# Kernel tuning notes

Hardware: AMD Instinct MI355X
Metric: run time of the kernel (lower is better)

The kernel has to match this reference:

```python
import jax, jax.numpy as jnp
import numpy as np

B, T, S, H, V = 4, 512, 1024, 768, 50257

def setup_inputs() -> dict:
    key = jax.random.key(0)
    k1, k2, k3, k4, k5, k6 = jax.random.split(key, 6)
    input_ids_to_copy = jax.random.randint(k1, (B, S), 0, V)
    cross_attentions = jax.random.uniform(k2, (B, T, S), dtype=jnp.float32)
    # normalize like attention weights
    cross_attentions = cross_attentions / jnp.sum(cross_attentions, axis=-1, keepdims=True)
    src_hidden_states = jax.random.normal(k3, (B, S, H), dtype=jnp.float32)
    tgt_hidden_states = jax.random.normal(k4, (B, T, H), dtype=jnp.float32)
    # p_gen_head = Linear(2H, 1) + Sigmoid
    W_pgen = jax.random.normal(k5, (2 * H, 1), dtype=jnp.float32) * (1.0 / np.sqrt(2 * H))
    b_pgen = jnp.zeros((1,), dtype=jnp.float32)
    return {
        "input_ids_to_copy": input_ids_to_copy,
        "cross_attentions": cross_attentions,
        "src_hidden_states": src_hidden_states,
        "tgt_hidden_states": tgt_hidden_states,
        "W_pgen": W_pgen,
        "b_pgen": b_pgen,
    }

def _copy_logits(attn_bts, ids_bs, vocab_size):
    # logits[b,t,v] = sum_s attn[b,t,s] * (ids[b,s] == v)
    # Efficient scatter-add over source positions instead of one-hot + matmul.
    def per_batch(attn_ts, ids_s):
        # attn_ts: [T,S], ids_s: [S] -> segment_sum over S -> [V,T] -> [T,V]
        return jax.ops.segment_sum(attn_ts.T, ids_s, num_segments=vocab_size).T
    return jax.vmap(per_batch)(attn_bts, ids_bs)

def reference(input_ids_to_copy, cross_attentions, src_hidden_states,
              tgt_hidden_states, W_pgen, b_pgen):
    # context_vectors: [B,T,H]
    context_vectors = jnp.einsum('bts,bsh->bth', cross_attentions, src_hidden_states)
    total_states = jnp.concatenate((context_vectors, tgt_hidden_states), axis=-1)  # [B,T,2H]
    p_gen = jax.nn.sigmoid(total_states @ W_pgen + b_pgen)  # [B,T,1]
    logits = _copy_logits(cross_attentions, input_ids_to_copy, V)  # [B,T,V]
    return (p_gen, logits)
```

## Files before the change

### kernel.cpp

```cpp
#include <hip/hip_runtime.h>
#include <hip/hip_bf16.h>
#include <math.h>

#define BB 4
#define TT 512
#define SS 1024
#define HH 768
#define VV 50257
#define NW 1571
#define NWP 1600
#define NPROJ 1536

__global__ __launch_bounds__(256) void prep_kernel(
    const float* __restrict__ src, const float* __restrict__ tgt,
    const float* __restrict__ W, const float* __restrict__ bptr,
    const int* __restrict__ ids,
    float* __restrict__ src_proj, float* __restrict__ tgt_proj,
    unsigned* __restrict__ bm_g, unsigned* __restrict__ pre_g,
    unsigned short* __restrict__ rank_g)
{
    __shared__ unsigned bm[NW];
    __shared__ unsigned pre[NW];
    __shared__ unsigned scan[256];
    const int tid = threadIdx.x;

    if (blockIdx.x < NPROJ) {
        const int wave = tid >> 6;
        const int lane = tid & 63;
        const int row  = blockIdx.x * 4 + wave;

        const float* vec;
        const float* w;
        if (row < BB * SS) { vec = src + (size_t)row * HH;            w = W; }
        else               { vec = tgt + (size_t)(row - BB*SS) * HH;  w = W + HH; }
        const float4* v4 = (const float4*)vec;
        const float4* w4 = (const float4*)w;

        float acc = 0.f;
#pragma unroll
        for (int k = 0; k < 3; ++k) {
            float4 a = v4[k * 64 + lane];
            float4 b = w4[k * 64 + lane];
            acc += a.x * b.x + a.y * b.y + a.z * b.z + a.w * b.w;
        }
#pragma unroll
        for (int off = 32; off > 0; off >>= 1) acc += __shfl_down(acc, off);
        if (lane == 0) {
            if (row < BB * SS) src_proj[row] = acc;
            else               tgt_proj[row - BB * SS] = acc + bptr[0];
        }
        return;
    }

    const int b = blockIdx.x - NPROJ;

    for (int i = tid; i < NW; i += 256) bm[i] = 0u;
    __syncthreads();
    const int* idb = ids + b * SS;
    for (int s = tid; s < SS; s += 256) {
        const int v = idb[s];
        atomicOr(&bm[v >> 5], 1u << (v & 31));
    }
    __syncthreads();

    unsigned cnt[7];
    unsigned local = 0;
    const int w0 = tid * 7;
#pragma unroll
    for (int k = 0; k < 7; ++k) {
        const int w = w0 + k;
        cnt[k] = local;
        local += (w < NW) ? (unsigned)__popc(bm[w]) : 0u;
    }
    scan[tid] = local;
    __syncthreads();
    for (int off = 1; off < 256; off <<= 1) {
        const unsigned mine = scan[tid];
        const unsigned add  = (tid >= off) ? scan[tid - off] : 0u;
        __syncthreads();
        scan[tid] = mine + add;
        __syncthreads();
    }
    const unsigned excl = (tid > 0) ? scan[tid - 1] : 0u;
#pragma unroll
    for (int k = 0; k < 7; ++k) {
        const int w = w0 + k;
        if (w < NW) {
            const unsigned p = excl + cnt[k];
            pre[w] = p;
            pre_g[b * NWP + w] = p;
            bm_g[b * NWP + w]  = bm[w];
        }
    }
    __syncthreads();
    for (int s = tid; s < SS; s += 256) {
        const int v = idb[s];
        const unsigned w = (unsigned)v >> 5, bit = (unsigned)v & 31u;
        const unsigned r = pre[w] + (unsigned)__popc(bm[w] & ((1u << bit) - 1u));
        rank_g[b * SS + s] = (unsigned short)r;
    }
}

__device__ __forceinline__ float lut1(int v, const unsigned* bm,
                                      const unsigned* pre, const float* vals)
{
    const unsigned w = bm[v >> 5];
    const unsigned bit = (unsigned)v & 31u;
    if ((w >> bit) & 1u)
        return vals[pre[v >> 5] + (unsigned)__popc(w & ((1u << bit) - 1u))];
    return 0.f;
}

__global__ __launch_bounds__(256) void row_kernel(
    const float* __restrict__ attn,
    const float* __restrict__ src_proj,
    const float* __restrict__ tgt_proj,
    const unsigned* __restrict__ bm_g,
    const unsigned* __restrict__ pre_g,
    const unsigned short* __restrict__ rank_g,
    float* __restrict__ out)
{
    __shared__ unsigned bm[NW];
    __shared__ unsigned pre[NW];
    __shared__ float vals[SS];
    __shared__ float wsum[4];

    const int row = blockIdx.x;
    const int b   = row >> 9;
    const int tid = threadIdx.x;

    for (int i = tid; i < NW; i += 256) { bm[i] = bm_g[b*NWP+i]; pre[i] = pre_g[b*NWP+i]; }
    ((float4*)vals)[tid] = make_float4(0.f, 0.f, 0.f, 0.f);
    __syncthreads();

    const float4*  a4p = (const float4*)(attn + (size_t)row * SS);
    const float4*  sp4 = (const float4*)(src_proj + b * SS);
    const ushort4* r4p = (const ushort4*)(rank_g + b * SS);
    const float4  a = a4p[tid];
    const float4  p = sp4[tid];
    const ushort4 r = r4p[tid];
    atomicAdd(&vals[r.x], a.x);
    atomicAdd(&vals[r.y], a.y);
    atomicAdd(&vals[r.z], a.z);
    atomicAdd(&vals[r.w], a.w);
    float acc = a.x * p.x + a.y * p.y + a.z * p.z + a.w * p.w;
#pragma unroll
    for (int off = 32; off > 0; off >>= 1) acc += __shfl_down(acc, off);
    if ((tid & 63) == 0) wsum[tid >> 6] = acc;
    __syncthreads();
    if (tid == 0) {
        const float x = wsum[0] + wsum[1] + wsum[2] + wsum[3] + tgt_proj[row];
        out[row] = 1.f / (1.f + expf(-x));
    }

    float* logits = out + (BB * TT) + (size_t)row * VV;
    const int head = (int)(((16u - (unsigned)((uintptr_t)logits & 15u)) & 15u) >> 2);
    if (tid < head) logits[tid] = lut1(tid, bm, pre, vals);

    const int n4 = (VV - head) >> 2;
    float4* p4 = (float4*)(logits + head);
    for (int i = tid; i < n4; i += 256) {
        const int v0 = head + (i << 2);
        float4 o = make_float4(0.f, 0.f, 0.f, 0.f);
        const unsigned w  = bm[v0 >> 5];
        const unsigned sh = (unsigned)v0 & 31u;
        unsigned nib;
        if (sh <= 28u) {
            nib = (w >> sh) & 0xFu;
        } else {
            const unsigned hi = bm[(v0 >> 5) + 1];
            nib = ((w >> sh) | (hi << (32u - sh))) & 0xFu;
        }
        if (nib) {
            o.x = lut1(v0,     bm, pre, vals);
            o.y = lut1(v0 + 1, bm, pre, vals);
            o.z = lut1(v0 + 2, bm, pre, vals);
            o.w = lut1(v0 + 3, bm, pre, vals);
        }
        p4[i] = o;
    }
    const int done = head + (n4 << 2);
    for (int v = done + tid; v < VV; v += 256)
        logits[v] = lut1(v, bm, pre, vals);
}

extern "C" void kernel_launch(void* const* d_in, const int* in_sizes, int n_in,
                              void* d_out, int out_size, void* d_ws, size_t ws_size,
                              hipStream_t stream) {
    const int*   ids  = (const int*)d_in[0];
    const float* attn = (const float*)d_in[1];
    const float* src  = (const float*)d_in[2];
    const float* tgt  = (const float*)d_in[3];
    const float* W    = (const float*)d_in[4];
    const float* bp   = (const float*)d_in[5];

    float* out = (float*)d_out;

    float*          src_proj = (float*)d_ws;
    float*          tgt_proj = src_proj + BB * SS;
    unsigned*       bm_g     = (unsigned*)(tgt_proj + BB * TT);
    unsigned*       pre_g    = bm_g + BB * NWP;
    unsigned short* rank_g   = (unsigned short*)(pre_g + BB * NWP);

    prep_kernel<<<NPROJ + BB, 256, 0, stream>>>(
        src, tgt, W, bp, ids, src_proj, tgt_proj, bm_g, pre_g, rank_g);
    row_kernel<<<BB * TT, 256, 0, stream>>>(
        attn, src_proj, tgt_proj, bm_g, pre_g, rank_g, out);
}
```

Before: 465.6 us.

## Zero-fill logit rows and scatter unique source values instead of dense LUT

Result: slower. 497.9 us (+6.9%).

```diff
diff --git a/kernel.cpp b/kernel.cpp
--- a/kernel.cpp
+++ b/kernel.cpp
@@ -1,5 +1,4 @@
 #include <hip/hip_runtime.h>
-#include <hip/hip_bf16.h>
 #include <math.h>
 
 #define BB 4
@@ -8,15 +7,14 @@
 #define HH 768
 #define VV 50257
 #define NW 1571
-#define NWP 1600
 #define NPROJ 1536
+#define NROWS (BB * TT)
 
 __global__ __launch_bounds__(256) void prep_kernel(
     const float* __restrict__ src, const float* __restrict__ tgt,
     const float* __restrict__ W, const float* __restrict__ bptr,
     const int* __restrict__ ids,
     float* __restrict__ src_proj, float* __restrict__ tgt_proj,
-    unsigned* __restrict__ bm_g, unsigned* __restrict__ pre_g,
     unsigned short* __restrict__ rank_g)
 {
     __shared__ unsigned bm[NW];
@@ -85,12 +83,7 @@
 #pragma unroll
     for (int k = 0; k < 7; ++k) {
         const int w = w0 + k;
-        if (w < NW) {
-            const unsigned p = excl + cnt[k];
-            pre[w] = p;
-            pre_g[b * NWP + w] = p;
-            bm_g[b * NWP + w]  = bm[w];
-        }
+        if (w < NW) pre[w] = excl + cnt[k];
     }
     __syncthreads();
     for (int s = tid; s < SS; s += 256) {
@@ -101,27 +94,14 @@
     }
 }
 
-__device__ __forceinline__ float lut1(int v, const unsigned* bm,
-                                      const unsigned* pre, const float* vals)
-{
-    const unsigned w = bm[v >> 5];
-    const unsigned bit = (unsigned)v & 31u;
-    if ((w >> bit) & 1u)
-        return vals[pre[v >> 5] + (unsigned)__popc(w & ((1u << bit) - 1u))];
-    return 0.f;
-}
-
 __global__ __launch_bounds__(256) void row_kernel(
     const float* __restrict__ attn,
     const float* __restrict__ src_proj,
     const float* __restrict__ tgt_proj,
-    const unsigned* __restrict__ bm_g,
-    const unsigned* __restrict__ pre_g,
     const unsigned short* __restrict__ rank_g,
+    const int* __restrict__ ids,
     float* __restrict__ out)
 {
-    __shared__ unsigned bm[NW];
-    __shared__ unsigned pre[NW];
     __shared__ float vals[SS];
     __shared__ float wsum[4];
 
@@ -129,16 +109,12 @@
     const int b   = row >> 9;
     const int tid = threadIdx.x;
 
-    for (int i = tid; i < NW; i += 256) { bm[i] = bm_g[b*NWP+i]; pre[i] = pre_g[b*NWP+i]; }
     ((float4*)vals)[tid] = make_float4(0.f, 0.f, 0.f, 0.f);
     __syncthreads();
 
-    const float4*  a4p = (const float4*)(attn + (size_t)row * SS);
-    const float4*  sp4 = (const float4*)(src_proj + b * SS);
-    const ushort4* r4p = (const ushort4*)(rank_g + b * SS);
-    const float4  a = a4p[tid];
-    const float4  p = sp4[tid];
-    const ushort4 r = r4p[tid];
+    const float4  a = ((const float4*)(attn + (size_t)row * SS))[tid];
+    const float4  p = ((const float4*)(src_proj + b * SS))[tid];
+    const ushort4 r = ((const ushort4*)(rank_g + b * SS))[tid];
     atomicAdd(&vals[r.x], a.x);
     atomicAdd(&vals[r.y], a.y);
     atomicAdd(&vals[r.z], a.z);
@@ -147,41 +123,35 @@
 #pragma unroll
     for (int off = 32; off > 0; off >>= 1) acc += __shfl_down(acc, off);
     if ((tid & 63) == 0) wsum[tid >> 6] = acc;
+
+    float* lp = out + NROWS + (size_t)row * VV;
+    const int h = (4 - (row & 3)) & 3;
+    if (tid < h) lp[tid] = 0.f;
+    float4* lp4 = (float4*)(lp + h);
+    const int n4 = (VV - h) >> 2;
+    const float4 z4 = make_float4(0.f, 0.f, 0.f, 0.f);
+    int i = tid;
+    for (; i + 768 < n4; i += 1024) {
+        lp4[i]       = z4;
+        lp4[i + 256] = z4;
+        lp4[i + 512] = z4;
+        lp4[i + 768] = z4;
+    }
+    for (; i < n4; i += 256) lp4[i] = z4;
+    const int t0 = h + (n4 << 2);
+    if (t0 + tid < VV) lp[t0 + tid] = 0.f;
+
     __syncthreads();
+
     if (tid == 0) {
         const float x = wsum[0] + wsum[1] + wsum[2] + wsum[3] + tgt_proj[row];
         out[row] = 1.f / (1.f + expf(-x));
     }
 
-    float* logits = out + (BB * TT) + (size_t)row * VV;
-    const int head = (int)(((16u - (unsigned)((uintptr_t)logits & 15u)) & 15u) >> 2);
-    if (tid < head) logits[tid] = lut1(tid, bm, pre, vals);
-
-    const int n4 = (VV - head) >> 2;
-    float4* p4 = (float4*)(logits + head);
-    for (int i = tid; i < n4; i += 256) {
-        const int v0 = head + (i << 2);
-        float4 o = make_float4(0.f, 0.f, 0.f, 0.f);
-        const unsigned w  = bm[v0 >> 5];
-        const unsigned sh = (unsigned)v0 & 31u;
-        unsigned nib;
-        if (sh <= 28u) {
-            nib = (w >> sh) & 0xFu;
-        } else {
-            const unsigned hi = bm[(v0 >> 5) + 1];
-            nib = ((w >> sh) | (hi << (32u - sh))) & 0xFu;
-        }
-        if (nib) {
-            o.x = lut1(v0,     bm, pre, vals);
-            o.y = lut1(v0 + 1, bm, pre, vals);
-            o.z = lut1(v0 + 2, bm, pre, vals);
-            o.w = lut1(v0 + 3, bm, pre, vals);
-        }
-        p4[i] = o;
-    }
-    const int done = head + (n4 << 2);
-    for (int v = done + tid; v < VV; v += 256)
-        logits[v] = lut1(v, bm, pre, vals);
+    const int*            idb = ids    + b * SS;
+    const unsigned short* rb  = rank_g + b * SS;
+    for (int s = tid; s < SS; s += 256)
+        lp[idb[s]] = vals[rb[s]];
 }
 
 extern "C" void kernel_launch(void* const* d_in, const int* in_sizes, int n_in,
@@ -198,12 +168,10 @@
 
     float*          src_proj = (float*)d_ws;
     float*          tgt_proj = src_proj + BB * SS;
-    unsigned*       bm_g     = (unsigned*)(tgt_proj + BB * TT);
-    unsigned*       pre_g    = bm_g + BB * NWP;
-    unsigned short* rank_g   = (unsigned short*)(pre_g + BB * NWP);
+    unsigned short* rank_g   = (unsigned short*)(tgt_proj + BB * TT);
 
     prep_kernel<<<NPROJ + BB, 256, 0, stream>>>(
-        src, tgt, W, bp, ids, src_proj, tgt_proj, bm_g, pre_g, rank_g);
-    row_kernel<<<BB * TT, 256, 0, stream>>>(
-        attn, src_proj, tgt_proj, bm_g, pre_g, rank_g, out);
+        src, tgt, W, bp, ids, src_proj, tgt_proj, rank_g);
+    row_kernel<<<NROWS, 256, 0, stream>>>(
+        attn, src_proj, tgt_proj, rank_g, ids, out);
 }
```
